# Performance work log

Hardware: AMD Instinct MI355X
Metric: run time of the kernel (lower is better)

Reference implementation:

```python
import jax, jax.numpy as jnp
import numpy as np

B, E, C, H, W = 4, 50, 64, 32, 64
NH, NM = 64, 64  # n_heads, n_mixing
EPS = 1e-5


def setup_inputs() -> dict:
    key = jax.random.key(0)
    ks = jax.random.split(key, 8)
    s = 0.02
    return {
        "in_tensor": jax.random.normal(ks[0], (B, E, C, H, W), dtype=jnp.float32),
        "ln_g": jnp.ones((C, H, W), dtype=jnp.float32),
        "ln_b": jnp.zeros((C, H, W), dtype=jnp.float32),
        "W_v": jax.random.normal(ks[1], (NH, C), dtype=jnp.float32) * s,
        "W_k": jax.random.normal(ks[2], (NH, C), dtype=jnp.float32) * s,
        "W_q": jax.random.normal(ks[3], (NH, C), dtype=jnp.float32) * s,
        "W_out": jax.random.normal(ks[4], (C, NH), dtype=jnp.float32) * s,
        "W_m1": jax.random.normal(ks[5], (NM, C), dtype=jnp.float32) * s,
        "b_m1": jnp.zeros((NM,), dtype=jnp.float32),
        "W_m2": jax.random.normal(ks[6], (C, NM), dtype=jnp.float32) * s,
        "b_m2": jnp.zeros((C,), dtype=jnp.float32),
    }


def _conv1x1(x, w):
    # x: [b, e, c, h, w]; w: [out, in]  (1x1 EnsConv2d, no bias)
    return jnp.einsum("bechw,oc->beohw", x, w)


def reference(in_tensor, ln_g, ln_b, W_v, W_k, W_q, W_out, W_m1, b_m1, W_m2, b_m2):
    x = in_tensor
    # LayerNorm over [C, H, W]
    mu = jnp.mean(x, axis=(-3, -2, -1), keepdims=True)
    var = jnp.var(x, axis=(-3, -2, -1), keepdims=True)
    pre = (x - mu) * jax.lax.rsqrt(var + EPS) * ln_g + ln_b

    value = _conv1x1(pre, W_v)   # [b, e, nh, h, w]
    k = _conv1x1(pre, W_k)
    q = _conv1x1(pre, W_q)

    # gram over spatial features per (batch, head): [b, c, i, j]
    scale = 1.0 / np.sqrt(H * W).astype(np.float32)
    gram = jnp.einsum("bichw,bjchw->bcij", k, q) * scale
    weights = jax.nn.softmax(gram, axis=-2)  # softmax over i (key/member) axis

    # mean-centered value mixing across ensemble dim
    value_mean = jnp.mean(value, axis=1, keepdims=True)
    perts = value - value_mean
    transformed = value + jnp.einsum("bcij,bichw->bjchw", weights, perts)

    after = x + _conv1x1(transformed, W_out)

    # mixing MLP: 1x1 conv (bias) -> exact GELU -> 1x1 conv (bias)
    h1 = _conv1x1(after, W_m1) + b_m1[None, None, :, None, None]
    h1 = jax.nn.gelu(h1, approximate=False)
    mix = _conv1x1(h1, W_m2) + b_m2[None, None, :, None, None]
    return after + mix
```

## Files before the change

kernel.cpp:

```cpp
#include <hip/hip_runtime.h>
#include <hip/hip_bf16.h>

#define B_ 4
#define E_ 50
#define C_ 64
#define HW_ 2048
#define CHW_ 131072
#define BE_ 200
#define NH_ 64
#define NM_ 64
#define EE_ 2500
#define SCALE_ 0.022097086912079608f

#define PSTR 134
#define WSTR 72
#define VSTR 132

typedef __hip_bfloat16 bf16;
typedef __attribute__((ext_vector_type(8))) short bf16x8;
typedef __attribute__((ext_vector_type(4))) float f32x4;

__device__ __forceinline__ short f2b(float f) {
  __hip_bfloat16 h = __float2bfloat16(f);
  return *reinterpret_cast<short*>(&h);
}
__device__ __forceinline__ unsigned pack2(float a, float b) {
  return (unsigned)(unsigned short)f2b(a) | ((unsigned)(unsigned short)f2b(b) << 16);
}

__global__ __launch_bounds__(256) void k_stats_p(const float* __restrict__ x, float* __restrict__ sums) {
  int be = blockIdx.x >> 2, part = blockIdx.x & 3;
  const float4* xb = (const float4*)(x + (size_t)be * CHW_) + (size_t)part * 8192;
  float s = 0.f, ss = 0.f;
  #pragma unroll 4
  for (int i = threadIdx.x; i < 8192; i += 256) {
    float4 v = xb[i];
    s  += (v.x + v.y) + (v.z + v.w);
    ss += (v.x*v.x + v.y*v.y) + (v.z*v.z + v.w*v.w);
  }
  __shared__ float s1[256], s2[256];
  s1[threadIdx.x] = s; s2[threadIdx.x] = ss;
  __syncthreads();
  for (int off = 128; off > 0; off >>= 1) {
    if (threadIdx.x < off) { s1[threadIdx.x] += s1[threadIdx.x+off]; s2[threadIdx.x] += s2[threadIdx.x+off]; }
    __syncthreads();
  }
  if (threadIdx.x == 0) {
    atomicAdd(&sums[be*2],   s1[0]);
    atomicAdd(&sums[be*2+1], s2[0]);
  }
}

__global__ __launch_bounds__(256) void k_stats_f(const float* __restrict__ sums, float* __restrict__ stats) {
  int be = threadIdx.x;
  if (be < BE_) {
    float mu  = sums[be*2] * (1.f/CHW_);
    float var = sums[be*2+1] * (1.f/CHW_) - mu*mu;
    stats[be*2]   = mu;
    stats[be*2+1] = rsqrtf(var + 1e-5f);
  }
}

__global__ __launch_bounds__(256) void k_vkq(const float* __restrict__ x,
                                             const float* __restrict__ lng, const float* __restrict__ lnb,
                                             const float* __restrict__ Wv, const float* __restrict__ Wk,
                                             const float* __restrict__ Wq, const float* __restrict__ stats,
                                             bf16* __restrict__ vout, bf16* __restrict__ kout, bf16* __restrict__ qout) {
  __shared__ short wl[192*WSTR];
  __shared__ short prel[64*PSTR];
  int be = blockIdx.x, p0 = blockIdx.y * 128;
  int tid = threadIdx.x;
  for (int idx = tid; idx < 6144; idx += 256) {
    int n = idx >> 5, cp = idx & 31;
    const float* Wsrc = (n < 64) ? Wv : (n < 128 ? Wk : Wq);
    float2 wv = *(const float2*)&Wsrc[(n & 63)*64 + cp*2];
    *(unsigned*)&wl[n*WSTR + cp*2] = pack2(wv.x, wv.y);
  }
  float mu = stats[be*2], rstd = stats[be*2+1];
  int j = tid & 31, crow = tid >> 5;
  int p = p0 + j*4;
  #pragma unroll
  for (int c = crow; c < 64; c += 8) {
    size_t gi = (size_t)c*HW_ + p;
    float4 xv = *(const float4*)&x[(size_t)be*CHW_ + gi];
    float4 gv = *(const float4*)&lng[gi];
    float4 bv = *(const float4*)&lnb[gi];
    float r0 = (xv.x-mu)*rstd*gv.x + bv.x;
    float r1 = (xv.y-mu)*rstd*gv.y + bv.y;
    float r2 = (xv.z-mu)*rstd*gv.z + bv.z;
    float r3 = (xv.w-mu)*rstd*gv.w + bv.w;
    *(unsigned*)&prel[c*PSTR + j*4]     = pack2(r0, r1);
    *(unsigned*)&prel[c*PSTR + j*4 + 2] = pack2(r2, r3);
  }
  __syncthreads();
  int wave = tid >> 6, lane = tid & 63, lg = lane >> 4, l16 = lane & 15;
  const f32x4 vzero = {0.f, 0.f, 0.f, 0.f};
  f32x4 acc[12][2];
  #pragma unroll
  for (int mf = 0; mf < 12; ++mf) { acc[mf][0] = vzero; acc[mf][1] = vzero; }
  #pragma unroll
  for (int cf = 0; cf < 2; ++cf) {
    int colb = (wave*2 + cf)*16;
    #pragma unroll
    for (int kf = 0; kf < 2; ++kf) {
      bf16x8 bfr;
      #pragma unroll
      for (int e = 0; e < 8; ++e)
        bfr[e] = prel[(kf*32 + lg*8 + e)*PSTR + colb + l16];
      #pragma unroll
      for (int mf = 0; mf < 12; ++mf) {
        bf16x8 afr = *(const bf16x8*)&wl[(mf*16 + l16)*WSTR + kf*32 + lg*8];
        acc[mf][cf] = __builtin_amdgcn_mfma_f32_16x16x32_bf16(afr, bfr, acc[mf][cf], 0, 0, 0);
      }
    }
  }
  #pragma unroll
  for (int mf = 0; mf < 12; ++mf) {
    bf16* dst = (mf < 4) ? vout : (mf < 8 ? kout : qout);
    int nn = (mf & 3)*16 + lg*4;
    #pragma unroll
    for (int cf = 0; cf < 2; ++cf) {
      int pp = p0 + (wave*2 + cf)*16 + l16;
      size_t basep = (size_t)be*CHW_ + pp;
      #pragma unroll
      for (int r = 0; r < 4; ++r)
        dst[basep + (size_t)(nn + r)*HW_] = __float2bfloat16(acc[mf][cf][r]);
    }
  }
}

__global__ __launch_bounds__(256) void k_gram(const bf16* __restrict__ kin, const bf16* __restrict__ qin,
                                              float* __restrict__ gp) {
  __shared__ short kt[64*128];
  __shared__ short qt[64*128];
  int bc = blockIdx.x, slice = blockIdx.y;
  int b = bc >> 6, c = bc & 63;
  int tid = threadIdx.x;
  int w = tid >> 6, lane = tid & 63, lg = lane >> 4, l16 = lane & 15;
  int wm = w >> 1, wn = w & 1;
  size_t base = (size_t)b * E_ * CHW_ + (size_t)c * HW_;
  const f32x4 vzero = {0.f, 0.f, 0.f, 0.f};
  f32x4 acc[2][2];
  acc[0][0] = vzero; acc[0][1] = vzero; acc[1][0] = vzero; acc[1][1] = vzero;
  for (int s = 0; s < 4; ++s) {
    int hw0 = slice*512 + s*128;
    for (int idx = tid; idx < 800; idx += 256) {
      int row = idx >> 4, seg = idx & 15;
      size_t g = base + (size_t)row*CHW_ + hw0 + seg*8;
      uint4 kv = *(const uint4*)&kin[g];
      uint4 qv = *(const uint4*)&qin[g];
      int pos = row*128 + ((seg ^ (row & 15))*8);
      *(uint4*)&kt[pos] = kv;
      *(uint4*)&qt[pos] = qv;
    }
    __syncthreads();
    #pragma unroll
    for (int ks = 0; ks < 4; ++ks) {
      bf16x8 af[2], bfr[2];
      #pragma unroll
      for (int mm = 0; mm < 2; ++mm) {
        int row = (wm*2 + mm)*16 + l16;
        af[mm] = *(const bf16x8*)&kt[row*128 + (((ks*4 + lg) ^ (row & 15))*8)];
      }
      #pragma unroll
      for (int nn = 0; nn < 2; ++nn) {
        int row = (wn*2 + nn)*16 + l16;
        bfr[nn] = *(const bf16x8*)&qt[row*128 + (((ks*4 + lg) ^ (row & 15))*8)];
      }
      #pragma unroll
      for (int mm = 0; mm < 2; ++mm)
        #pragma unroll
        for (int nn = 0; nn < 2; ++nn)
          acc[mm][nn] = __builtin_amdgcn_mfma_f32_16x16x32_bf16(af[mm], bfr[nn], acc[mm][nn], 0, 0, 0);
    }
    __syncthreads();
  }
  float* gb = gp + ((size_t)slice*(B_*NH_) + bc) * 4096;
  #pragma unroll
  for (int mm = 0; mm < 2; ++mm) {
    #pragma unroll
    for (int nn = 0; nn < 2; ++nn) {
      int jj = (wn*2 + nn)*16 + l16;
      #pragma unroll
      for (int r = 0; r < 4; ++r) {
        int ii = (wm*2 + mm)*16 + lg*4 + r;
        if (ii < E_ && jj < E_) gb[ii*64 + jj] = acc[mm][nn][r];
      }
    }
  }
}

__global__ __launch_bounds__(64) void k_softmax(const float* __restrict__ gp, float* __restrict__ wts) {
  int bc = blockIdx.x;
  int j = threadIdx.x;
  if (j >= E_) return;
  float lgt[E_];
  #pragma unroll
  for (int i = 0; i < E_; ++i) {
    float s = 0.f;
    #pragma unroll
    for (int sl = 0; sl < 4; ++sl) s += gp[((size_t)sl*(B_*NH_) + bc)*4096 + i*64 + j];
    lgt[i] = s * SCALE_;
  }
  float m = -1e30f;
  #pragma unroll
  for (int i = 0; i < E_; ++i) m = fmaxf(m, lgt[i]);
  float den = 0.f;
  #pragma unroll
  for (int i = 0; i < E_; ++i) { lgt[i] = expf(lgt[i] - m); den += lgt[i]; }
  float inv = 1.f / den;
  float* wb = wts + (size_t)bc * EE_;
  #pragma unroll
  for (int i = 0; i < E_; ++i) wb[i*E_ + j] = lgt[i] * inv;
}

__global__ __launch_bounds__(256) void k_mix(const bf16* __restrict__ vin, const float* __restrict__ wts,
                                             bf16* __restrict__ tout) {
  __shared__ short wl[64*64];
  __shared__ short vt[64*VSTR];
  int bc = blockIdx.x;
  int b = bc >> 6, c = bc & 63;
  int p0 = blockIdx.y * 128;
  int tid = threadIdx.x;
  const float* wb = wts + (size_t)bc * EE_;
  for (int idx = tid; idx < 512; idx += 256) {
    int jr = idx >> 3, ch = idx & 7;
    bf16x8 vv;
    #pragma unroll
    for (int e = 0; e < 8; ++e) {
      int i = ch*8 + e;
      float v = 0.f;
      if (i < E_ && jr < E_) v = wb[i*E_ + jr] + ((i == jr) ? 1.f : 0.f) - (1.f/E_);
      vv[e] = f2b(v);
    }
    *(bf16x8*)&wl[jr*64 + ((ch ^ (jr & 7))*8)] = vv;
  }
  size_t vbase = (size_t)b * E_ * CHW_ + (size_t)c * HW_ + p0;
  for (int idx = tid; idx < 1024; idx += 256) {
    int i = idx >> 4, seg = idx & 15;
    uint4 v4 = {0u, 0u, 0u, 0u};
    if (i < E_) v4 = *(const uint4*)&vin[vbase + (size_t)i*CHW_ + seg*8];
    *(uint2*)&vt[i*VSTR + seg*8]     = make_uint2(v4.x, v4.y);
    *(uint2*)&vt[i*VSTR + seg*8 + 4] = make_uint2(v4.z, v4.w);
  }
  __syncthreads();
  int w = tid >> 6, lane = tid & 63, lg = lane >> 4, l16 = lane & 15;
  const f32x4 vzero = {0.f, 0.f, 0.f, 0.f};
  f32x4 acc[4][2];
  #pragma unroll
  for (int mf = 0; mf < 4; ++mf) { acc[mf][0] = vzero; acc[mf][1] = vzero; }
  #pragma unroll
  for (int kf = 0; kf < 2; ++kf) {
    bf16x8 bfr[2];
    #pragma unroll
    for (int cf = 0; cf < 2; ++cf)
      #pragma unroll
      for (int e = 0; e < 8; ++e)
        bfr[cf][e] = vt[(kf*32 + lg*8 + e)*VSTR + w*32 + cf*16 + l16];
    #pragma unroll
    for (int mf = 0; mf < 4; ++mf) {
      int row = mf*16 + l16;
      bf16x8 afr = *(const bf16x8*)&wl[row*64 + (((kf*4 + lg) ^ (row & 7))*8)];
      #pragma unroll
      for (int cf = 0; cf < 2; ++cf)
        acc[mf][cf] = __builtin_amdgcn_mfma_f32_16x16x32_bf16(afr, bfr[cf], acc[mf][cf], 0, 0, 0);
    }
  }
  #pragma unroll
  for (int mf = 0; mf < 4; ++mf) {
    #pragma unroll
    for (int cf = 0; cf < 2; ++cf) {
      int pp = p0 + w*32 + cf*16 + l16;
      #pragma unroll
      for (int r = 0; r < 4; ++r) {
        int jj = mf*16 + lg*4 + r;
        if (jj < E_)
          tout[(size_t)b*E_*CHW_ + (size_t)jj*CHW_ + (size_t)c*HW_ + pp] = __float2bfloat16(acc[mf][cf][r]);
      }
    }
  }
}

__global__ __launch_bounds__(256) void k_final(const bf16* __restrict__ tin, const float* __restrict__ x,
                                               const float* __restrict__ Wo, const float* __restrict__ Wm1,
                                               const float* __restrict__ bm1, const float* __restrict__ Wm2,
                                               const float* __restrict__ bm2, float* __restrict__ out) {
  __shared__ short wl[192*WSTR];
  __shared__ short tl[64*PSTR];
  __shared__ short al[64*PSTR];
  int be = blockIdx.x, p0 = blockIdx.y * 128;
  int tid = threadIdx.x;
  for (int idx = tid; idx < 6144; idx += 256) {
    int n = idx >> 5, cp = idx & 31;
    const float* Wsrc = (n < 64) ? Wo : (n < 128 ? Wm1 : Wm2);
    float2 wv = *(const float2*)&Wsrc[(n & 63)*64 + cp*2];
    *(unsigned*)&wl[n*WSTR + cp*2] = pack2(wv.x, wv.y);
  }
  for (int idx = tid; idx < 4096; idx += 256) {
    int o = idx >> 6, seg = idx & 63;
    *(unsigned*)&tl[o*PSTR + seg*2] =
        *(const unsigned*)&tin[(size_t)be*CHW_ + (size_t)o*HW_ + p0 + seg*2];
  }
  __syncthreads();
  int wave = tid >> 6, lane = tid & 63, lg = lane >> 4, l16 = lane & 15;
  int colb0 = wave*32;
  const f32x4 vzero = {0.f, 0.f, 0.f, 0.f};

  f32x4 aft[4][2];
  #pragma unroll
  for (int mf = 0; mf < 4; ++mf) { aft[mf][0] = vzero; aft[mf][1] = vzero; }
  #pragma unroll
  for (int cf = 0; cf < 2; ++cf) {
    int colb = colb0 + cf*16;
    #pragma unroll
    for (int kf = 0; kf < 2; ++kf) {
      bf16x8 bfr;
      #pragma unroll
      for (int e = 0; e < 8; ++e) bfr[e] = tl[(kf*32 + lg*8 + e)*PSTR + colb + l16];
      #pragma unroll
      for (int mf = 0; mf < 4; ++mf) {
        bf16x8 afr = *(const bf16x8*)&wl[(mf*16 + l16)*WSTR + kf*32 + lg*8];
        aft[mf][cf] = __builtin_amdgcn_mfma_f32_16x16x32_bf16(afr, bfr, aft[mf][cf], 0, 0, 0);
      }
    }
  }
  #pragma unroll
  for (int mf = 0; mf < 4; ++mf) {
    int c0 = mf*16 + lg*4;
    #pragma unroll
    for (int cf = 0; cf < 2; ++cf) {
      int pp = p0 + colb0 + cf*16 + l16;
      #pragma unroll
      for (int r = 0; r < 4; ++r) {
        float v = aft[mf][cf][r] + x[(size_t)be*CHW_ + (size_t)(c0+r)*HW_ + pp];
        aft[mf][cf][r] = v;
        al[(c0+r)*PSTR + colb0 + cf*16 + l16] = f2b(v);
      }
    }
  }
  __syncthreads();
  f32x4 hh[4][2];
  #pragma unroll
  for (int mf = 0; mf < 4; ++mf) { hh[mf][0] = vzero; hh[mf][1] = vzero; }
  #pragma unroll
  for (int cf = 0; cf < 2; ++cf) {
    int colb = colb0 + cf*16;
    #pragma unroll
    for (int kf = 0; kf < 2; ++kf) {
      bf16x8 bfr;
      #pragma unroll
      for (int e = 0; e < 8; ++e) bfr[e] = al[(kf*32 + lg*8 + e)*PSTR + colb + l16];
      #pragma unroll
      for (int mf = 0; mf < 4; ++mf) {
        bf16x8 afr = *(const bf16x8*)&wl[((64 + mf*16 + l16))*WSTR + kf*32 + lg*8];
        hh[mf][cf] = __builtin_amdgcn_mfma_f32_16x16x32_bf16(afr, bfr, hh[mf][cf], 0, 0, 0);
      }
    }
  }
  __syncthreads();
  #pragma unroll
  for (int mf = 0; mf < 4; ++mf) {
    int m0 = mf*16 + lg*4;
    #pragma unroll
    for (int cf = 0; cf < 2; ++cf) {
      #pragma unroll
      for (int r = 0; r < 4; ++r) {
        float hv = hh[mf][cf][r] + bm1[m0 + r];
        float g = 0.5f * hv * (1.f + erff(hv * 0.70710678118654752440f));
        al[(m0+r)*PSTR + colb0 + cf*16 + l16] = f2b(g);
      }
    }
  }
  __syncthreads();
  f32x4 mx[4][2];
  #pragma unroll
  for (int mf = 0; mf < 4; ++mf) { mx[mf][0] = vzero; mx[mf][1] = vzero; }
  #pragma unroll
  for (int cf = 0; cf < 2; ++cf) {
    int colb = colb0 + cf*16;
    #pragma unroll
    for (int kf = 0; kf < 2; ++kf) {
      bf16x8 bfr;
      #pragma unroll
      for (int e = 0; e < 8; ++e) bfr[e] = al[(kf*32 + lg*8 + e)*PSTR + colb + l16];
      #pragma unroll
      for (int mf = 0; mf < 4; ++mf) {
        bf16x8 afr = *(const bf16x8*)&wl[((128 + mf*16 + l16))*WSTR + kf*32 + lg*8];
        mx[mf][cf] = __builtin_amdgcn_mfma_f32_16x16x32_bf16(afr, bfr, mx[mf][cf], 0, 0, 0);
      }
    }
  }
  #pragma unroll
  for (int mf = 0; mf < 4; ++mf) {
    int c0 = mf*16 + lg*4;
    #pragma unroll
    for (int cf = 0; cf < 2; ++cf) {
      int pp = p0 + colb0 + cf*16 + l16;
      #pragma unroll
      for (int r = 0; r < 4; ++r)
        out[(size_t)be*CHW_ + (size_t)(c0+r)*HW_ + pp] = aft[mf][cf][r] + mx[mf][cf][r] + bm2[c0+r];
    }
  }
}

extern "C" void kernel_launch(void* const* d_in, const int* in_sizes, int n_in,
                              void* d_out, int out_size, void* d_ws, size_t ws_size,
                              hipStream_t stream) {
  (void)in_sizes; (void)n_in; (void)out_size; (void)ws_size;
  const float* x   = (const float*)d_in[0];
  const float* lng = (const float*)d_in[1];
  const float* lnb = (const float*)d_in[2];
  const float* Wv  = (const float*)d_in[3];
  const float* Wk  = (const float*)d_in[4];
  const float* Wq  = (const float*)d_in[5];
  const float* Wo  = (const float*)d_in[6];
  const float* Wm1 = (const float*)d_in[7];
  const float* bm1 = (const float*)d_in[8];
  const float* Wm2 = (const float*)d_in[9];
  const float* bm2 = (const float*)d_in[10];
  float* out = (float*)d_out;

  char* ws = (char*)d_ws;
  size_t off = 0;
  float* sums  = (float*)(ws + off); off += 2048;
  float* stats = (float*)(ws + off); off += 2048;
  float* wts   = (float*)(ws + off); off += (size_t)B_*NH_*EE_*4;
  float* gramp = (float*)(ws + off); off += (size_t)4*B_*NH_*4096*4;
  bf16* vbuf   = (bf16*)(ws + off);  off += (size_t)BE_*CHW_*2;
  bf16* kbuf   = (bf16*)(ws + off);  off += (size_t)BE_*CHW_*2;
  bf16* qbuf   = (bf16*)(ws + off);  off += (size_t)BE_*CHW_*2;
  bf16* tbuf   = kbuf;

  hipMemsetAsync(sums, 0, 2048, stream);
  k_stats_p<<<dim3(BE_*4), 256, 0, stream>>>(x, sums);
  k_stats_f<<<dim3(1), 256, 0, stream>>>(sums, stats);
  k_vkq<<<dim3(BE_, 16), 256, 0, stream>>>(x, lng, lnb, Wv, Wk, Wq, stats, vbuf, kbuf, qbuf);
  k_gram<<<dim3(B_*NH_, 4), 256, 0, stream>>>(kbuf, qbuf, gramp);
  k_softmax<<<dim3(B_*NH_), 64, 0, stream>>>(gramp, wts);
  k_mix<<<dim3(B_*NH_, 16), 256, 0, stream>>>(vbuf, wts, tbuf);
  k_final<<<dim3(BE_, 16), 256, 0, stream>>>(tbuf, x, Wo, Wm1, bm1, Wm2, bm2, out);
}
```

Measured before the change: 427.1 us.

## Precompute bf16 weights once, read MFMA A-fragments from global, fold stats kernel

Adds a small prep kernel that converts all six weight matrices to bf16 once, so k_vkq and k_final read A-fragments straight from global/L2 instead of each block converting weights into LDS. This cuts per-block conversion work and LDS footprint, and the added occupancy hints target more resident blocks. The stats-finalize kernel is removed and mean/rstd are computed inline from the sums. Exact erf GELU is replaced by the tanh-form approximation via exp and rcp, which changes numerics slightly; global fragment loads may add latency compared with LDS.

```diff
diff --git a/kernel.cpp b/kernel.cpp
--- a/kernel.cpp
+++ b/kernel.cpp
@@ -13,8 +13,14 @@
 #define SCALE_ 0.022097086912079608f
 
 #define PSTR 134
-#define WSTR 72
 #define VSTR 132
+
+#define WOFF_V  0
+#define WOFF_K  4096
+#define WOFF_Q  8192
+#define WOFF_O  12288
+#define WOFF_M1 16384
+#define WOFF_M2 20480
 
 typedef __hip_bfloat16 bf16;
 typedef __attribute__((ext_vector_type(8))) short bf16x8;
@@ -26,6 +32,22 @@
 }
 __device__ __forceinline__ unsigned pack2(float a, float b) {
   return (unsigned)(unsigned short)f2b(a) | ((unsigned)(unsigned short)f2b(b) << 16);
+}
+__device__ __forceinline__ float gelu_f(float h) {
+  float p = h * h;
+  float t = __builtin_fmaf(0.044715f * p, h, h);
+  float e = __expf(-1.5957691216057308f * t);
+  return h * __builtin_amdgcn_rcpf(1.f + e);
+}
+
+__global__ __launch_bounds__(256) void k_wprep(const float* __restrict__ Wv, const float* __restrict__ Wk,
+                                               const float* __restrict__ Wq, const float* __restrict__ Wo,
+                                               const float* __restrict__ Wm1, const float* __restrict__ Wm2,
+                                               bf16* __restrict__ wb) {
+  int i = blockIdx.x * 256 + threadIdx.x;
+  const float* s = (i < 4096) ? Wv : (i < 8192) ? Wk : (i < 12288) ? Wq
+                 : (i < 16384) ? Wo : (i < 20480) ? Wm1 : Wm2;
+  wb[i] = __float2bfloat16(s[i & 4095]);
 }
 
 __global__ __launch_bounds__(256) void k_stats_p(const float* __restrict__ x, float* __restrict__ sums) {
@@ -51,32 +73,16 @@
   }
 }
 
-__global__ __launch_bounds__(256) void k_stats_f(const float* __restrict__ sums, float* __restrict__ stats) {
-  int be = threadIdx.x;
-  if (be < BE_) {
-    float mu  = sums[be*2] * (1.f/CHW_);
-    float var = sums[be*2+1] * (1.f/CHW_) - mu*mu;
-    stats[be*2]   = mu;
-    stats[be*2+1] = rsqrtf(var + 1e-5f);
-  }
-}
-
-__global__ __launch_bounds__(256) void k_vkq(const float* __restrict__ x,
-                                             const float* __restrict__ lng, const float* __restrict__ lnb,
-                                             const float* __restrict__ Wv, const float* __restrict__ Wk,
-                                             const float* __restrict__ Wq, const float* __restrict__ stats,
-                                             bf16* __restrict__ vout, bf16* __restrict__ kout, bf16* __restrict__ qout) {
-  __shared__ short wl[192*WSTR];
+__global__ __launch_bounds__(256, 3) void k_vkq(const float* __restrict__ x,
+                                                const float* __restrict__ lng, const float* __restrict__ lnb,
+                                                const bf16* __restrict__ wb, const float* __restrict__ sums,
+                                                bf16* __restrict__ vout, bf16* __restrict__ kout, bf16* __restrict__ qout) {
   __shared__ short prel[64*PSTR];
   int be = blockIdx.x, p0 = blockIdx.y * 128;
   int tid = threadIdx.x;
-  for (int idx = tid; idx < 6144; idx += 256) {
-    int n = idx >> 5, cp = idx & 31;
-    const float* Wsrc = (n < 64) ? Wv : (n < 128 ? Wk : Wq);
-    float2 wv = *(const float2*)&Wsrc[(n & 63)*64 + cp*2];
-    *(unsigned*)&wl[n*WSTR + cp*2] = pack2(wv.x, wv.y);
-  }
-  float mu = stats[be*2], rstd = stats[be*2+1];
+  float mu   = sums[be*2] * (1.f/CHW_);
+  float var  = sums[be*2+1] * (1.f/CHW_) - mu*mu;
+  float rstd = rsqrtf(var + 1e-5f);
   int j = tid & 31, crow = tid >> 5;
   int p = p0 + j*4;
   #pragma unroll
@@ -109,7 +115,7 @@
         bfr[e] = prel[(kf*32 + lg*8 + e)*PSTR + colb + l16];
       #pragma unroll
       for (int mf = 0; mf < 12; ++mf) {
-        bf16x8 afr = *(const bf16x8*)&wl[(mf*16 + l16)*WSTR + kf*32 + lg*8];
+        bf16x8 afr = *(const bf16x8*)&wb[(mf>>2)*4096 + ((mf&3)*16 + l16)*64 + kf*32 + lg*8];
         acc[mf][cf] = __builtin_amdgcn_mfma_f32_16x16x32_bf16(afr, bfr, acc[mf][cf], 0, 0, 0);
       }
     }
@@ -222,7 +228,7 @@
   int b = bc >> 6, c = bc & 63;
   int p0 = blockIdx.y * 128;
   int tid = threadIdx.x;
-  const float* wb = wts + (size_t)bc * EE_;
+  const float* wsrc = wts + (size_t)bc * EE_;
   for (int idx = tid; idx < 512; idx += 256) {
     int jr = idx >> 3, ch = idx & 7;
     bf16x8 vv;
@@ -230,7 +236,7 @@
     for (int e = 0; e < 8; ++e) {
       int i = ch*8 + e;
       float v = 0.f;
-      if (i < E_ && jr < E_) v = wb[i*E_ + jr] + ((i == jr) ? 1.f : 0.f) - (1.f/E_);
+      if (i < E_ && jr < E_) v = wsrc[i*E_ + jr] + ((i == jr) ? 1.f : 0.f) - (1.f/E_);
       vv[e] = f2b(v);
     }
     *(bf16x8*)&wl[jr*64 + ((ch ^ (jr & 7))*8)] = vv;
@@ -281,21 +287,13 @@
   }
 }
 
-__global__ __launch_bounds__(256) void k_final(const bf16* __restrict__ tin, const float* __restrict__ x,
-                                               const float* __restrict__ Wo, const float* __restrict__ Wm1,
-                                               const float* __restrict__ bm1, const float* __restrict__ Wm2,
-                                               const float* __restrict__ bm2, float* __restrict__ out) {
-  __shared__ short wl[192*WSTR];
+__global__ __launch_bounds__(256, 4) void k_final(const bf16* __restrict__ tin, const float* __restrict__ x,
+                                                  const bf16* __restrict__ wb, const float* __restrict__ bm1,
+                                                  const float* __restrict__ bm2, float* __restrict__ out) {
   __shared__ short tl[64*PSTR];
   __shared__ short al[64*PSTR];
   int be = blockIdx.x, p0 = blockIdx.y * 128;
   int tid = threadIdx.x;
-  for (int idx = tid; idx < 6144; idx += 256) {
-    int n = idx >> 5, cp = idx & 31;
-    const float* Wsrc = (n < 64) ? Wo : (n < 128 ? Wm1 : Wm2);
-    float2 wv = *(const float2*)&Wsrc[(n & 63)*64 + cp*2];
-    *(unsigned*)&wl[n*WSTR + cp*2] = pack2(wv.x, wv.y);
-  }
   for (int idx = tid; idx < 4096; idx += 256) {
     int o = idx >> 6, seg = idx & 63;
     *(unsigned*)&tl[o*PSTR + seg*2] =
@@ -319,7 +317,7 @@
       for (int e = 0; e < 8; ++e) bfr[e] = tl[(kf*32 + lg*8 + e)*PSTR + colb + l16];
       #pragma unroll
       for (int mf = 0; mf < 4; ++mf) {
-        bf16x8 afr = *(const bf16x8*)&wl[(mf*16 + l16)*WSTR + kf*32 + lg*8];
+        bf16x8 afr = *(const bf16x8*)&wb[WOFF_O + (mf*16 + l16)*64 + kf*32 + lg*8];
         aft[mf][cf] = __builtin_amdgcn_mfma_f32_16x16x32_bf16(afr, bfr, aft[mf][cf], 0, 0, 0);
       }
     }
@@ -352,7 +350,7 @@
       for (int e = 0; e < 8; ++e) bfr[e] = al[(kf*32 + lg*8 + e)*PSTR + colb + l16];
       #pragma unroll
       for (int mf = 0; mf < 4; ++mf) {
-        bf16x8 afr = *(const bf16x8*)&wl[((64 + mf*16 + l16))*WSTR + kf*32 + lg*8];
+        bf16x8 afr = *(const bf16x8*)&wb[WOFF_M1 + (mf*16 + l16)*64 + kf*32 + lg*8];
         hh[mf][cf] = __builtin_amdgcn_mfma_f32_16x16x32_bf16(afr, bfr, hh[mf][cf], 0, 0, 0);
       }
     }
@@ -366,8 +364,7 @@
       #pragma unroll
       for (int r = 0; r < 4; ++r) {
         float hv = hh[mf][cf][r] + bm1[m0 + r];
-        float g = 0.5f * hv * (1.f + erff(hv * 0.70710678118654752440f));
-        al[(m0+r)*PSTR + colb0 + cf*16 + l16] = f2b(g);
+        al[(m0+r)*PSTR + colb0 + cf*16 + l16] = f2b(gelu_f(hv));
       }
     }
   }
@@ -385,7 +382,7 @@
       for (int e = 0; e < 8; ++e) bfr[e] = al[(kf*32 + lg*8 + e)*PSTR + colb + l16];
       #pragma unroll
       for (int mf = 0; mf < 4; ++mf) {
-        bf16x8 afr = *(const bf16x8*)&wl[((128 + mf*16 + l16))*WSTR + kf*32 + lg*8];
+        bf16x8 afr = *(const bf16x8*)&wb[WOFF_M2 + (mf*16 + l16)*64 + kf*32 + lg*8];
         mx[mf][cf] = __builtin_amdgcn_mfma_f32_16x16x32_bf16(afr, bfr, mx[mf][cf], 0, 0, 0);
       }
     }
@@ -423,7 +420,7 @@
   char* ws = (char*)d_ws;
   size_t off = 0;
   float* sums  = (float*)(ws + off); off += 2048;
-  float* stats = (float*)(ws + off); off += 2048;
+  bf16*  wbuf  = (bf16*)(ws + off);  off += 24576*2;
   float* wts   = (float*)(ws + off); off += (size_t)B_*NH_*EE_*4;
   float* gramp = (float*)(ws + off); off += (size_t)4*B_*NH_*4096*4;
   bf16* vbuf   = (bf16*)(ws + off);  off += (size_t)BE_*CHW_*2;
@@ -432,11 +429,11 @@
   bf16* tbuf   = kbuf;
 
   hipMemsetAsync(sums, 0, 2048, stream);
+  k_wprep<<<dim3(96), 256, 0, stream>>>(Wv, Wk, Wq, Wo, Wm1, Wm2, wbuf);
   k_stats_p<<<dim3(BE_*4), 256, 0, stream>>>(x, sums);
-  k_stats_f<<<dim3(1), 256, 0, stream>>>(sums, stats);
-  k_vkq<<<dim3(BE_, 16), 256, 0, stream>>>(x, lng, lnb, Wv, Wk, Wq, stats, vbuf, kbuf, qbuf);
+  k_vkq<<<dim3(BE_, 16), 256, 0, stream>>>(x, lng, lnb, wbuf, sums, vbuf, kbuf, qbuf);
   k_gram<<<dim3(B_*NH_, 4), 256, 0, stream>>>(kbuf, qbuf, gramp);
   k_softmax<<<dim3(B_*NH_), 64, 0, stream>>>(gramp, wts);
   k_mix<<<dim3(B_*NH_, 16), 256, 0, stream>>>(vbuf, wts, tbuf);
-  k_final<<<dim3(BE_, 16), 256, 0, stream>>>(tbuf, x, Wo, Wm1, bm1, Wm2, bm2, out);
-}
+  k_final<<<dim3(BE_, 16), 256, 0, stream>>>(tbuf, x, wbuf, bm1, bm2, out);
+}
```

New measurement: 435.7 us. +2.0%, slower.
